# Optimization experiments

Measured on AMD Instinct MI355X. Metric: run time of the kernel, lower is better.

Reference implementation:

```python
import jax, jax.numpy as jnp
import numpy as np

NUM_GROUPS = 8
INPUT_DIM = 1024
OUTPUT_DIM = 1024
TOKENS_PER_GROUP = 8192  # rows per group after reshape


def setup_inputs() -> dict:
    key = jax.random.key(0)
    kx, kw = jax.random.split(key)
    # x: [N*G, D_in] as fed to the torch module (it reshapes internally)
    x = jax.random.normal(kx, (TOKENS_PER_GROUP * NUM_GROUPS, INPUT_DIM), dtype=jnp.float32)
    # Stacked per-group Linear weights, torch layout [D_out, D_in] per group.
    # Xavier-normal gain=1: std = sqrt(2 / (fan_in + fan_out))
    std = np.sqrt(2.0 / (INPUT_DIM + OUTPUT_DIM)).astype(np.float32)
    W = jax.random.normal(kw, (NUM_GROUPS, OUTPUT_DIM, INPUT_DIM), dtype=jnp.float32) * std
    return {"x": x, "W": W}


def reference(x, W):
    # x: [N*G, D_in] -> [N, G, D_in]
    n = x.shape[0] // NUM_GROUPS
    xg = x.reshape(n, NUM_GROUPS, INPUT_DIM)
    # per-group linear: out[n,g,k] = sum_d xg[n,g,d] * W[g,k,d]
    out = jnp.einsum("ngd,gkd->ngk", xg, W)
    return out.reshape(-1, OUTPUT_DIM)
```

## Files before the change

### kernel.cpp

```cpp
#include <hip/hip_runtime.h>
#include <hip/hip_bf16.h>


namespace {

constexpr int NG   = 8;
constexpr int DIN  = 1024;
constexpr int DOUT = 1024;
constexpr int BM   = 128;
constexpr int BN   = 256;
constexpr int BK   = 32;
constexpr int NKT  = DIN / BK;
constexpr int AROWB = BK * 4;
constexpr int BROWB = BK * 2;
constexpr int ATILE = BM * AROWB;
constexpr int BTILE = BN * BROWB;
constexpr int LDS_BYTES = 2 * ATILE + 2 * BTILE;
constexpr int JTN  = DOUT / BN;
constexpr size_t WSB_BYTES = (size_t)NG * JTN * NKT * BTILE;

typedef __attribute__((ext_vector_type(8))) short bf16x8;
typedef __attribute__((ext_vector_type(4))) float f32x4;

__device__ __forceinline__ bf16x8 pack_bf16x8v(f32x4 lo, f32x4 hi) {
  union { __hip_bfloat162 h2[4]; bf16x8 v; } p;
  p.h2[0] = __float22bfloat162_rn(make_float2(lo.x, lo.y));
  p.h2[1] = __float22bfloat162_rn(make_float2(lo.z, lo.w));
  p.h2[2] = __float22bfloat162_rn(make_float2(hi.x, hi.y));
  p.h2[3] = __float22bfloat162_rn(make_float2(hi.z, hi.w));
  return p.v;
}

__device__ __forceinline__ void glds16(const void* g, void* l) {
  __builtin_amdgcn_global_load_lds(
      (const __attribute__((address_space(1))) unsigned int*)g,
      (__attribute__((address_space(3))) unsigned int*)l, 16, 0, 0);
}

#define FENCE() asm volatile("" ::: "memory")
#define BAR()   do { FENCE(); __builtin_amdgcn_s_barrier(); FENCE(); } while (0)
#define LGKM0() asm volatile("s_waitcnt lgkmcnt(0)" ::: "memory")
#define VM0()   asm volatile("s_waitcnt vmcnt(0)" ::: "memory")
#define MFMA_(a, b, c) __builtin_amdgcn_mfma_f32_16x16x32_bf16((a), (b), (c), 0, 0, 0)

__global__ __launch_bounds__(256)
void cvt_w_kernel(const float* __restrict__ W, char* __restrict__ wsB) {
  const int q    = (int)blockIdx.x * 256 + (int)threadIdx.x;
  const int tile = q >> 10;
  const int r    = (q & 1023) >> 2;
  const int w    = q & 3;
  const int g    = tile >> 7;
  const int jt   = (tile >> 5) & 3;
  const int kt   = tile & 31;

  const float* src = W + (size_t)(g * DOUT + jt * BN + r) * DIN
                       + kt * BK + ((w ^ (r & 3)) * 8);
  f32x4 lo = *(const f32x4*)(src);
  f32x4 hi = *(const f32x4*)(src + 4);
  *(bf16x8*)(wsB + (size_t)q * 16) = pack_bf16x8v(lo, hi);
}

template <bool WSB>
__global__ __launch_bounds__(512, 4)
void gemm_k(const float* __restrict__ X, const float* __restrict__ W,
            const char* __restrict__ wsB, float* __restrict__ O) {
  extern __shared__ char smem[];
  char* const smA = smem;
  char* const smB = smem + 2 * ATILE;

  const int bid = (int)blockIdx.x;
  const int swz = (bid & 7) * 256 + (bid >> 3);
  const int jt = swz & 3;
  const int it = (swz >> 2) & 63;
  const int g  = swz >> 8;

  const int n0 = it * BM;
  const int c0 = jt * BN;

  const int tid  = (int)threadIdx.x;
  const int lane = tid & 63;
  const int wid  = tid >> 6;
  const int wr   = wid >> 2;
  const int wc   = wid & 3;
  const int fr   = lane & 15;
  const int fq   = lane >> 4;

  const int aR = tid >> 3;
  const int aw = (tid & 7) ^ (aR & 7);
  const char* aSrc0 = (const char*)X
      + ((size_t)(n0 + aR) * NG + g) * (DIN * 4) + aw * 16;
  const char* aSrc1 = aSrc0 + (size_t)64 * NG * DIN * 4;

  const char* BgT = wsB + (size_t)((g * JTN + jt) * NKT) * BTILE;
  const int s_l = tid & 3;
  const int s_r = tid >> 2;
  const float* Bg = W + (size_t)g * DOUT * DIN + (size_t)(c0 + s_r) * DIN
                      + s_l * 8;
  const int bw0 = s_r * BROWB + ((s_l ^ (s_r & 3)) * 16);

  const int gA0   = (2 * fq) ^ (fr & 7);
  const int aoff0 = (wr * 64 + fr) * AROWB + gA0 * 16;
  const int aoff1 = (wr * 64 + fr) * AROWB + (gA0 ^ 1) * 16;
  const int boff  = (wc * 64 + fr) * BROWB + ((fq ^ (fr & 3)) * 16);

  f32x4 acc[4][4];
#pragma unroll
  for (int m = 0; m < 4; ++m)
#pragma unroll
    for (int n = 0; n < 4; ++n) acc[m][n] = (f32x4){0.f, 0.f, 0.f, 0.f};

  glds16(aSrc0, smA + tid * 16);
  glds16(aSrc1, smA + 8192 + tid * 16);
  if (WSB) {
    glds16(BgT + tid * 16, smB + tid * 16);
    glds16(BgT + 8192 + tid * 16, smB + 8192 + tid * 16);
  } else {
    f32x4 b0 = *(const f32x4*)(Bg);
    f32x4 b1 = *(const f32x4*)(Bg + 4);
    f32x4 b2 = *(const f32x4*)(Bg + (size_t)128 * DIN);
    f32x4 b3 = *(const f32x4*)(Bg + (size_t)128 * DIN + 4);
    *(bf16x8*)(smB + bw0)        = pack_bf16x8v(b0, b1);
    *(bf16x8*)(smB + 8192 + bw0) = pack_bf16x8v(b2, b3);
    LGKM0();
  }
  VM0();
  BAR();

  for (int t = 0; t < NKT; ++t) {
    char* const cA = smA + (t & 1) * ATILE;
    char* const cB = smB + (t & 1) * BTILE;
    char* const nA = smA + ((t & 1) ^ 1) * ATILE;
    char* const nB = smB + ((t & 1) ^ 1) * BTILE;
    const bool stage = (t + 1) < NKT;

    f32x4 bS0, bS1, bS2, bS3;
    if (stage) {
      glds16(aSrc0 + (size_t)(t + 1) * (BK * 4), nA + tid * 16);
      glds16(aSrc1 + (size_t)(t + 1) * (BK * 4), nA + 8192 + tid * 16);
      if (WSB) {
        const char* Bn = BgT + (size_t)(t + 1) * BTILE;
        glds16(Bn + tid * 16, nB + tid * 16);
        glds16(Bn + 8192 + tid * 16, nB + 8192 + tid * 16);
      } else {
        const float* Bn = Bg + (size_t)(t + 1) * BK;
        bS0 = *(const f32x4*)(Bn);
        bS1 = *(const f32x4*)(Bn + 4);
        bS2 = *(const f32x4*)(Bn + (size_t)128 * DIN);
        bS3 = *(const f32x4*)(Bn + (size_t)128 * DIN + 4);
      }
    }

    bf16x8 bfr[4];
#pragma unroll
    for (int n = 0; n < 4; ++n)
      bfr[n] = *(const bf16x8*)(cB + boff + n * 1024);

    __builtin_amdgcn_s_setprio(1);
#pragma unroll
    for (int m = 0; m < 4; ++m) {
      f32x4 lo = *(const f32x4*)(cA + aoff0 + m * 2048);
      f32x4 hi = *(const f32x4*)(cA + aoff1 + m * 2048);
      bf16x8 am = pack_bf16x8v(lo, hi);
#pragma unroll
      for (int n = 0; n < 4; ++n)
        acc[m][n] = MFMA_(am, bfr[n], acc[m][n]);
    }
    __builtin_amdgcn_s_setprio(0);

    if (!WSB && stage) {
      *(bf16x8*)(nB + bw0)        = pack_bf16x8v(bS0, bS1);
      *(bf16x8*)(nB + 8192 + bw0) = pack_bf16x8v(bS2, bS3);
      LGKM0();
    }
    if (stage) { VM0(); BAR(); }
  }

#pragma unroll
  for (int m = 0; m < 4; ++m) {
#pragma unroll
    for (int r = 0; r < 4; ++r) {
      const int row = wr * 64 + m * 16 + fq * 4 + r;
      float* orow = O + ((size_t)(n0 + row) * NG + g) * DOUT + c0 + wc * 64;
#pragma unroll
      for (int n = 0; n < 4; ++n) {
        orow[n * 16 + fr] = acc[m][n][r];
      }
    }
  }
}

}

extern "C" void kernel_launch(void* const* d_in, const int* in_sizes, int n_in,
                              void* d_out, int out_size, void* d_ws, size_t ws_size,
                              hipStream_t stream) {
  (void)n_in; (void)out_size;
  const float* X = (const float*)d_in[0];
  const float* W = (const float*)d_in[1];
  float* O = (float*)d_out;

  const int tokens_total = in_sizes[0] / DIN;
  const int ntok_per_g   = tokens_total / NG;
  const int grid = NG * (ntok_per_g / BM) * (DOUT / BN);

  if (ws_size >= WSB_BYTES) {
    const int cvt_grid = (int)(WSB_BYTES / 16 / 256);
    cvt_w_kernel<<<dim3(cvt_grid), dim3(256), 0, stream>>>(W, (char*)d_ws);
    (void)hipFuncSetAttribute((const void*)gemm_k<true>,
                              hipFuncAttributeMaxDynamicSharedMemorySize,
                              LDS_BYTES);
    gemm_k<true><<<dim3(grid), dim3(512), LDS_BYTES, stream>>>(
        X, W, (const char*)d_ws, O);
  } else {
    (void)hipFuncSetAttribute((const void*)gemm_k<false>,
                              hipFuncAttributeMaxDynamicSharedMemorySize,
                              LDS_BYTES);
    gemm_k<false><<<dim3(grid), dim3(512), LDS_BYTES, stream>>>(
        X, W, nullptr, O);
  }
}
```

Measured before the change: 224.3 us.

## Convert X tiles to bf16 in registers before LDS with two-deep prefetch

The A operand (X) is now loaded from global memory into registers two k-steps ahead, converted to bf16 and stored to LDS. Previously it was copied as fp32 straight into LDS and converted on every fragment read. This halves A's LDS footprint and read traffic, removes the per-MFMA conversion from the inner loop, and switches to static shared memory with a new XOR swizzle shared by A and B. The loop is unrolled by two with a partial vmcnt wait. In exchange it adds register pressure for the staged fp32 data and VALU conversion work after the MFMAs, which may hurt occupancy at launch bound 512x4.

Result: slower. 230.5 us (+2.8%).

```diff
diff --git a/kernel.cpp b/kernel.cpp
--- a/kernel.cpp
+++ b/kernel.cpp
@@ -11,11 +11,9 @@
 constexpr int BN   = 256;
 constexpr int BK   = 32;
 constexpr int NKT  = DIN / BK;
-constexpr int AROWB = BK * 4;
-constexpr int BROWB = BK * 2;
-constexpr int ATILE = BM * AROWB;
-constexpr int BTILE = BN * BROWB;
-constexpr int LDS_BYTES = 2 * ATILE + 2 * BTILE;
+constexpr int ROWB  = BK * 2;
+constexpr int ATILE = BM * ROWB;
+constexpr int BTILE = BN * ROWB;
 constexpr int JTN  = DOUT / BN;
 constexpr size_t WSB_BYTES = (size_t)NG * JTN * NKT * BTILE;
 
@@ -41,32 +39,90 @@
 #define BAR()   do { FENCE(); __builtin_amdgcn_s_barrier(); FENCE(); } while (0)
 #define LGKM0() asm volatile("s_waitcnt lgkmcnt(0)" ::: "memory")
 #define VM0()   asm volatile("s_waitcnt vmcnt(0)" ::: "memory")
+#define VMC2()  asm volatile("s_waitcnt vmcnt(2)" ::: "memory")
 #define MFMA_(a, b, c) __builtin_amdgcn_mfma_f32_16x16x32_bf16((a), (b), (c), 0, 0, 0)
 
 __global__ __launch_bounds__(256)
 void cvt_w_kernel(const float* __restrict__ W, char* __restrict__ wsB) {
   const int q    = (int)blockIdx.x * 256 + (int)threadIdx.x;
   const int tile = q >> 10;
-  const int r    = (q & 1023) >> 2;
-  const int w    = q & 3;
+  const int qi   = q & 1023;
+  const int r    = qi >> 2;
+  const int w    = qi & 3;
   const int g    = tile >> 7;
   const int jt   = (tile >> 5) & 3;
   const int kt   = tile & 31;
 
   const float* src = W + (size_t)(g * DOUT + jt * BN + r) * DIN
-                       + kt * BK + ((w ^ (r & 3)) * 8);
+                       + kt * BK + ((w ^ ((r >> 1) & 3)) * 8);
   f32x4 lo = *(const f32x4*)(src);
   f32x4 hi = *(const f32x4*)(src + 4);
   *(bf16x8*)(wsB + (size_t)q * 16) = pack_bf16x8v(lo, hi);
 }
+
+#define KBODY(T, CUR)                                                          \
+  {                                                                            \
+    const int t_ = (T);                                                        \
+    char* const cA = smA + (CUR) * ATILE;                                      \
+    char* const cB = smB + (CUR) * BTILE;                                      \
+    char* const nA = smA + (1 - (CUR)) * ATILE;                                \
+    char* const nB = smB + (1 - (CUR)) * BTILE;                                \
+    const bool st1 = (t_ + 1) < NKT;                                           \
+    const bool st2 = (t_ + 2) < NKT;                                           \
+    if (WSB) {                                                                 \
+      if (st1) {        \
+        const char* Bn = BgT + (size_t)(t_ + 1) * BTILE;                       \
+        glds16(Bn + tid * 16, nB + tid * 16);                                  \
+        glds16(Bn + 8192 + tid * 16, nB + 8192 + tid * 16);                    \
+      }                                                                        \
+      FENCE();                                                                 \
+    }                                                                          \
+    if (st2) {                         \
+      const float* An = aSrc + (size_t)(t_ + 2) * BK;                          \
+      aS[CUR][0] = *(const f32x4*)(An);                                        \
+      aS[CUR][1] = *(const f32x4*)(An + 4);                                    \
+    }                                                                          \
+    if (!WSB && st1) {                                                         \
+      const float* Bn = bSrc + (size_t)(t_ + 1) * BK;                          \
+      bS[0] = *(const f32x4*)(Bn);                                             \
+      bS[1] = *(const f32x4*)(Bn + 4);                                         \
+      bS[2] = *(const f32x4*)(Bn + (size_t)128 * DIN);                         \
+      bS[3] = *(const f32x4*)(Bn + (size_t)128 * DIN + 4);                     \
+    }                                                                          \
+    FENCE();                                                                   \
+    bf16x8 bfr[4];                                                             \
+    _Pragma("unroll")                                                          \
+    for (int n = 0; n < 4; ++n)                                                \
+      bfr[n] = *(const bf16x8*)(cB + boff + n * 1024);                         \
+    __builtin_amdgcn_s_setprio(1);                                             \
+    _Pragma("unroll")                                                          \
+    for (int m = 0; m < 4; ++m) {                                              \
+      bf16x8 am = *(const bf16x8*)(cA + aoff + m * 1024);                      \
+      _Pragma("unroll")                                                        \
+      for (int n = 0; n < 4; ++n)                                              \
+        acc[m][n] = MFMA_(am, bfr[n], acc[m][n]);                              \
+    }                                                                          \
+    __builtin_amdgcn_s_setprio(0);                                             \
+    if (st1) {                                                                 \
+       \
+      *(bf16x8*)(nA + tid * 16) = pack_bf16x8v(aS[1 - (CUR)][0],               \
+                                               aS[1 - (CUR)][1]);              \
+      if (!WSB) {                                                              \
+        *(bf16x8*)(nB + tid * 16)        = pack_bf16x8v(bS[0], bS[1]);         \
+        *(bf16x8*)(nB + tid * 16 + 8192) = pack_bf16x8v(bS[2], bS[3]);         \
+      }                                                                        \
+      LGKM0();                                                                 \
+      if (WSB) { if (st2) { VMC2(); } else { VM0(); } }                        \
+      BAR();                                                                   \
+    }                                                                          \
+  }
 
 template <bool WSB>
 __global__ __launch_bounds__(512, 4)
 void gemm_k(const float* __restrict__ X, const float* __restrict__ W,
             const char* __restrict__ wsB, float* __restrict__ O) {
-  extern __shared__ char smem[];
-  char* const smA = smem;
-  char* const smB = smem + 2 * ATILE;
+  __shared__ __align__(16) char smA[2 * ATILE];
+  __shared__ __align__(16) char smB[2 * BTILE];
 
   const int bid = (int)blockIdx.x;
   const int swz = (bid & 7) * 256 + (bid >> 3);
@@ -85,94 +141,56 @@
   const int fr   = lane & 15;
   const int fq   = lane >> 4;
 
-  const int aR = tid >> 3;
-  const int aw = (tid & 7) ^ (aR & 7);
-  const char* aSrc0 = (const char*)X
-      + ((size_t)(n0 + aR) * NG + g) * (DIN * 4) + aw * 16;
-  const char* aSrc1 = aSrc0 + (size_t)64 * NG * DIN * 4;
+  {
+  }
+  const int aRow = tid >> 2;
+  const int aChk = (tid & 3) ^ ((tid >> 3) & 3);
+  const float* aSrc = X + ((size_t)(n0 + aRow) * NG + g) * DIN + aChk * 8;
 
   const char* BgT = wsB + (size_t)((g * JTN + jt) * NKT) * BTILE;
-  const int s_l = tid & 3;
-  const int s_r = tid >> 2;
-  const float* Bg = W + (size_t)g * DOUT * DIN + (size_t)(c0 + s_r) * DIN
-                      + s_l * 8;
-  const int bw0 = s_r * BROWB + ((s_l ^ (s_r & 3)) * 16);
-
-  const int gA0   = (2 * fq) ^ (fr & 7);
-  const int aoff0 = (wr * 64 + fr) * AROWB + gA0 * 16;
-  const int aoff1 = (wr * 64 + fr) * AROWB + (gA0 ^ 1) * 16;
-  const int boff  = (wc * 64 + fr) * BROWB + ((fq ^ (fr & 3)) * 16);
-
+  const int bRow = tid >> 2;
+  const int bChk = (tid & 3) ^ ((tid >> 3) & 3);
+  const float* bSrc = W + (size_t)(g * DOUT + c0 + bRow) * DIN + bChk * 8;
+
+  const int psw  = (fq ^ ((fr >> 1) & 3)) << 4;
+  const int aoff = (wr * 64 + fr) * ROWB + psw;
+  const int boff = (wc * 64 + fr) * ROWB + psw;
+
+  f32x4 aS[2][2];
+  f32x4 bS[4];
   f32x4 acc[4][4];
 #pragma unroll
   for (int m = 0; m < 4; ++m)
 #pragma unroll
     for (int n = 0; n < 4; ++n) acc[m][n] = (f32x4){0.f, 0.f, 0.f, 0.f};
 
-  glds16(aSrc0, smA + tid * 16);
-  glds16(aSrc1, smA + 8192 + tid * 16);
+  aS[0][0] = *(const f32x4*)(aSrc);
+  aS[0][1] = *(const f32x4*)(aSrc + 4);
   if (WSB) {
     glds16(BgT + tid * 16, smB + tid * 16);
     glds16(BgT + 8192 + tid * 16, smB + 8192 + tid * 16);
   } else {
-    f32x4 b0 = *(const f32x4*)(Bg);
-    f32x4 b1 = *(const f32x4*)(Bg + 4);
-    f32x4 b2 = *(const f32x4*)(Bg + (size_t)128 * DIN);
-    f32x4 b3 = *(const f32x4*)(Bg + (size_t)128 * DIN + 4);
-    *(bf16x8*)(smB + bw0)        = pack_bf16x8v(b0, b1);
-    *(bf16x8*)(smB + 8192 + bw0) = pack_bf16x8v(b2, b3);
-    LGKM0();
-  }
-  VM0();
+    bS[0] = *(const f32x4*)(bSrc);
+    bS[1] = *(const f32x4*)(bSrc + 4);
+    bS[2] = *(const f32x4*)(bSrc + (size_t)128 * DIN);
+    bS[3] = *(const f32x4*)(bSrc + (size_t)128 * DIN + 4);
+  }
+  FENCE();
+  aS[1][0] = *(const f32x4*)(aSrc + BK);
+  aS[1][1] = *(const f32x4*)(aSrc + BK + 4);
+  FENCE();
+  *(bf16x8*)(smA + tid * 16) = pack_bf16x8v(aS[0][0], aS[0][1]);
+  if (!WSB) {
+    *(bf16x8*)(smB + tid * 16)        = pack_bf16x8v(bS[0], bS[1]);
+    *(bf16x8*)(smB + tid * 16 + 8192) = pack_bf16x8v(bS[2], bS[3]);
+  }
+  LGKM0();
+  if (WSB) { VMC2(); }
   BAR();
 
-  for (int t = 0; t < NKT; ++t) {
-    char* const cA = smA + (t & 1) * ATILE;
-    char* const cB = smB + (t & 1) * BTILE;
-    char* const nA = smA + ((t & 1) ^ 1) * ATILE;
-    char* const nB = smB + ((t & 1) ^ 1) * BTILE;
-    const bool stage = (t + 1) < NKT;
-
-    f32x4 bS0, bS1, bS2, bS3;
-    if (stage) {
-      glds16(aSrc0 + (size_t)(t + 1) * (BK * 4), nA + tid * 16);
-      glds16(aSrc1 + (size_t)(t + 1) * (BK * 4), nA + 8192 + tid * 16);
-      if (WSB) {
-        const char* Bn = BgT + (size_t)(t + 1) * BTILE;
-        glds16(Bn + tid * 16, nB + tid * 16);
-        glds16(Bn + 8192 + tid * 16, nB + 8192 + tid * 16);
-      } else {
-        const float* Bn = Bg + (size_t)(t + 1) * BK;
-        bS0 = *(const f32x4*)(Bn);
-        bS1 = *(const f32x4*)(Bn + 4);
-        bS2 = *(const f32x4*)(Bn + (size_t)128 * DIN);
-        bS3 = *(const f32x4*)(Bn + (size_t)128 * DIN + 4);
-      }
-    }
-
-    bf16x8 bfr[4];
-#pragma unroll
-    for (int n = 0; n < 4; ++n)
-      bfr[n] = *(const bf16x8*)(cB + boff + n * 1024);
-
-    __builtin_amdgcn_s_setprio(1);
-#pragma unroll
-    for (int m = 0; m < 4; ++m) {
-      f32x4 lo = *(const f32x4*)(cA + aoff0 + m * 2048);
-      f32x4 hi = *(const f32x4*)(cA + aoff1 + m * 2048);
-      bf16x8 am = pack_bf16x8v(lo, hi);
-#pragma unroll
-      for (int n = 0; n < 4; ++n)
-        acc[m][n] = MFMA_(am, bfr[n], acc[m][n]);
-    }
-    __builtin_amdgcn_s_setprio(0);
-
-    if (!WSB && stage) {
-      *(bf16x8*)(nB + bw0)        = pack_bf16x8v(bS0, bS1);
-      *(bf16x8*)(nB + 8192 + bw0) = pack_bf16x8v(bS2, bS3);
-      LGKM0();
-    }
-    if (stage) { VM0(); BAR(); }
+  for (int tt = 0; tt < NKT; tt += 2) {
+    KBODY(tt, 0);
+    KBODY(tt + 1, 1);
   }
 
 #pragma unroll
@@ -206,16 +224,10 @@
   if (ws_size >= WSB_BYTES) {
     const int cvt_grid = (int)(WSB_BYTES / 16 / 256);
     cvt_w_kernel<<<dim3(cvt_grid), dim3(256), 0, stream>>>(W, (char*)d_ws);
-    (void)hipFuncSetAttribute((const void*)gemm_k<true>,
-                              hipFuncAttributeMaxDynamicSharedMemorySize,
-                              LDS_BYTES);
-    gemm_k<true><<<dim3(grid), dim3(512), LDS_BYTES, stream>>>(
+    gemm_k<true><<<dim3(grid), dim3(512), 0, stream>>>(
         X, W, (const char*)d_ws, O);
   } else {
-    (void)hipFuncSetAttribute((const void*)gemm_k<false>,
-                              hipFuncAttributeMaxDynamicSharedMemorySize,
-                              LDS_BYTES);
-    gemm_k<false><<<dim3(grid), dim3(512), LDS_BYTES, stream>>>(
+    gemm_k<false><<<dim3(grid), dim3(512), 0, stream>>>(
         X, W, nullptr, O);
   }
 }
```
